# Optimization experiments

Measured on AMD Instinct MI355X. Metric: run time of the kernel, lower is better.

## Reference

```python
import jax, jax.numpy as jnp
import numpy as np
from jax import lax

LAM = 1.0   # risk.distance calls wasserstein with lam=1
ITS = 20    # and its=20
EPS_K = 1e-6


def setup_inputs() -> dict:
    key = jax.random.key(0)
    k1, k2 = jax.random.split(key)
    N, S, D = 4096, 32, 128
    X_ls = jax.random.normal(k1, (N, S, D), dtype=jnp.float32)
    t = jax.random.randint(k2, (N,), 0, 2).astype(jnp.int32)
    return {"X_ls": X_ls, "t": t}


def _pdist2sq(X, Y):
    # squared Euclidean distance between all pairs: [nt, nc]
    C = -2.0 * (X @ Y.T)
    nx = jnp.sum(jnp.square(X), axis=1, keepdims=True)   # [nt,1]
    ny = jnp.sum(jnp.square(Y), axis=1, keepdims=True)   # [nc,1]
    return C + ny.T + nx


def _sinkhorn_step(Xt, Xc, p, lam, its):
    # Xt: [nt, d], Xc: [nc, d]  -> scalar 2*sum(T*Mt)
    nt = jnp.float32(Xt.shape[0])
    nc = jnp.float32(Xc.shape[0])
    M = _pdist2sq(Xt, Xc)                                   # [nt, nc]
    delta = lax.stop_gradient(jnp.max(M))
    eff_lam = lax.stop_gradient(lam / jnp.mean(M))
    # augmented cost matrix Mt: [nt+1, nc+1]
    row = delta * jnp.ones((1, M.shape[1]), M.dtype)
    col = jnp.concatenate([delta * jnp.ones((M.shape[0], 1), M.dtype),
                           jnp.zeros((1, 1), M.dtype)], axis=0)
    Mt = jnp.concatenate([jnp.concatenate([M, row], axis=0), col], axis=1)
    # marginals a: [nt+1,1], b: [nc+1,1]
    a = jnp.concatenate([(p / nt) * jnp.ones((Xt.shape[0], 1), M.dtype),
                         (1.0 - p) * jnp.ones((1, 1), M.dtype)], axis=0)
    b = jnp.concatenate([((1.0 - p) / nc) * jnp.ones((Xc.shape[0], 1), M.dtype),
                         p * jnp.ones((1, 1), M.dtype)], axis=0)
    K = jnp.exp(-eff_lam * Mt) + EPS_K
    ainvK = K / a
    def body(i, u):
        # u^T K -> transpose -> K^T u : [nc+1,1]
        return 1.0 / (ainvK @ (b / (K.T @ u)))
    u = lax.fori_loop(0, its, body, a)
    v = b / (K.T @ u)                                       # [nc+1,1]
    T = u * (v.T * K)                                       # [nt+1, nc+1]
    T = lax.stop_gradient(T)                                # backpropT=False
    return 2.0 * jnp.sum(T * Mt)


def _wasserstein(X_ls, t, lam=LAM, its=ITS):
    # Data-dependent split on treatment (concrete, eager) — matches tf.where+gather.
    t_np = np.asarray(t)
    it_idx = np.nonzero(t_np > 0)[0]
    ic_idx = np.nonzero(t_np < 1)[0]
    p = jnp.float32(t_np.astype(np.float32).mean())          # p_t = np.mean(t)
    Xt_all = jnp.transpose(X_ls[it_idx], (1, 0, 2))          # [S, nt, d]
    Xc_all = jnp.transpose(X_ls[ic_idx], (1, 0, 2))          # [S, nc, d]
    per_step = jax.vmap(lambda Xt, Xc: _sinkhorn_step(Xt, Xc, p, lam, its))
    return jnp.sum(per_step(Xt_all, Xc_all))                 # sum over timesteps


def reference(X_ls, t):
    return _wasserstein(X_ls, t)
```

## Files before the change

### kernel.cpp

```cpp
#include <hip/hip_runtime.h>
#include <stdint.h>

typedef unsigned char u8;
typedef unsigned short u16;
typedef uint32_t u32;

#define NTOT 4096
#define SS   32
#define DD   128
#define EPSK 1e-6f
#define NITER 20
#define CAPC 4460544u
#define LDC_FIT 2304
#define WSTR 2432
#define SU_OFF 2308
#define UNT_OFF 2309
#define BPT 16

typedef __attribute__((ext_vector_type(8))) short short8;
typedef __attribute__((ext_vector_type(4))) float f32x4;
typedef __attribute__((ext_vector_type(2))) float f32x2;

__device__ __forceinline__ float bf2f(u16 h){ return __uint_as_float(((u32)h) << 16); }
__device__ __forceinline__ u16 f2bf(float f){
  u32 u = __float_as_uint(f);
  u += 0x7fffu + ((u >> 16) & 1u);
  return (u16)(u >> 16);
}
__device__ __forceinline__ int invpermc(int cp){
  return (cp & ~63) | ((cp & 3) << 4) | ((cp >> 2) & 15);
}

__global__ __launch_bounds__(1024) void k_compact(const int* __restrict__ t,
    int* __restrict__ itidx, int* __restrict__ icidx, int* __restrict__ meta,
    float* __restrict__ fmeta)
{
  __shared__ int sc[1024];
  int tid = threadIdx.x;
  int e0 = tid * 4;
  int tv[4]; int c = 0;
  #pragma unroll
  for (int e = 0; e < 4; e++){ tv[e] = t[e0 + e]; c += (tv[e] > 0) ? 1 : 0; }
  sc[tid] = c;
  __syncthreads();
  for (int off = 1; off < 1024; off <<= 1){
    int v = sc[tid];
    int add = (tid >= off) ? sc[tid - off] : 0;
    __syncthreads();
    sc[tid] = v + add;
    __syncthreads();
  }
  int incl = sc[tid];
  int excl = incl - c;
  int oT = excl, oC = e0 - excl;
  #pragma unroll
  for (int e = 0; e < 4; e++){
    if (tv[e] > 0) itidx[oT++] = e0 + e;
    else           icidx[oC++] = e0 + e;
  }
  if (tid == 1023){
    meta[0] = incl; meta[1] = NTOT - incl;
    fmeta[0] = (float)incl / (float)NTOT;
  }
}

__global__ void k_zero(float* __restrict__ p, int n)
{
  int i = blockIdx.x * 256 + threadIdx.x;
  if (i < n) p[i] = 0.f;
}

__global__ void k_vinit(const float* __restrict__ fmeta, float* __restrict__ w0)
{
  if (threadIdx.x == 0){
    float p = fmeta[0];
    float* w = w0 + (size_t)blockIdx.x * WSTR;
    w[SU_OFF]  = p;
    w[UNT_OFF] = 1.0f - p;
  }
}

__global__ __launch_bounds__(256) void k_pack(const float* __restrict__ X,
    const int* __restrict__ itidx, const int* __restrict__ icidx,
    const int* __restrict__ meta, u16* __restrict__ XT, u16* __restrict__ XC,
    float* __restrict__ nxT, float* __restrict__ nxC, int ts0)
{
  int r = blockIdx.x * 256 + threadIdx.x;
  int isC = blockIdx.y;
  int z = blockIdx.z;
  int s = ts0 + z;
  int n = isC ? meta[1] : meta[0];
  if (r >= n) return;
  int idx = isC ? icidx[r] : itidx[r];
  const float4* src = (const float4*)(X + ((size_t)idx * SS + s) * DD);
  u16* dst = (isC ? XC : XT) + ((size_t)z * NTOT + r) * DD;
  float nrm = 0.f;
  #pragma unroll
  for (int q = 0; q < 32; q++){
    float4 v = src[q];
    nrm += v.x*v.x + v.y*v.y + v.z*v.z + v.w*v.w;
    u32 lo = (u32)f2bf(v.x) | ((u32)f2bf(v.y) << 16);
    u32 hi = (u32)f2bf(v.z) | ((u32)f2bf(v.w) << 16);
    uint2 pk; pk.x = lo; pk.y = hi;
    ((uint2*)dst)[q] = pk;
  }
  (isC ? nxC : nxT)[z * NTOT + r] = nrm;
}

__global__ __launch_bounds__(256) void k_stats(const u16* __restrict__ XT,
    const u16* __restrict__ XC, const float* __restrict__ nxT, const float* __restrict__ nxC,
    const int* __restrict__ meta, float* __restrict__ gsx, float* __restrict__ gsn)
{
  int side = blockIdx.y, z = blockIdx.z;
  int n = side ? meta[1] : meta[0];
  int chunk = (n + 7) >> 3;
  int r0 = blockIdx.x * chunk;
  int r1 = min(r0 + chunk, n);
  const u16* B = (side ? XC : XT) + (size_t)z * NTOT * DD;
  int tid = threadIdx.x;
  int d = tid & 127, half = tid >> 7;
  float sx = 0.f;
  for (int r = r0 + half; r < r1; r += 2) sx += bf2f(B[(size_t)r * DD + d]);
  __shared__ float sp[256];
  sp[tid] = sx;
  __syncthreads();
  if (tid < 128) unsafeAtomicAdd(&gsx[(size_t)(z*2+side)*128 + tid], sp[tid] + sp[tid+128]);
  const float* nrm = (side ? nxC : nxT) + (size_t)z * NTOT;
  float sn = 0.f;
  for (int r = r0 + tid; r < r1; r += 256) sn += nrm[r];
  #pragma unroll
  for (int o = 32; o; o >>= 1) sn += __shfl_xor(sn, o);
  __syncthreads();
  if ((tid & 63) == 0) sp[tid >> 6] = sn;
  __syncthreads();
  if (tid == 0) unsafeAtomicAdd(&gsn[z*2+side], sp[0]+sp[1]+sp[2]+sp[3]);
}

__global__ void k_lam(const float* __restrict__ gsx, const float* __restrict__ gsn,
                      const int* __restrict__ meta, float* __restrict__ stats)
{
  int z = blockIdx.x, tid = threadIdx.x;
  float d = gsx[(size_t)(z*2)*128 + tid] * gsx[(size_t)(z*2+1)*128 + tid];
  #pragma unroll
  for (int o = 32; o; o >>= 1) d += __shfl_xor(d, o);
  __shared__ float rr[2];
  if ((tid & 63) == 0) rr[tid >> 6] = d;
  __syncthreads();
  if (tid == 0){
    float nt = (float)meta[0], nc = (float)meta[1];
    float msum = nc * gsn[z*2] + nt * gsn[z*2+1] - 2.f * (rr[0] + rr[1]);
    stats[z*8+0] = nt * nc / msum;
    stats[z*8+1] = msum / (nt * nc);
  }
}

#define LDA2 72
__global__ __launch_bounds__(256) void k_gemm(const u16* __restrict__ XT,
    const u16* __restrict__ XC, const float* __restrict__ nxT, const float* __restrict__ nxC,
    const int* __restrict__ meta, const float* __restrict__ fmeta,
    float* __restrict__ stats, u8* __restrict__ Kc, float* __restrict__ w0base)
{
  int nt = meta[0], nc = meta[1];
  if (nt > LDC_FIT || nc > LDC_FIT) return;
  int bx = blockIdx.x, by = blockIdx.y, z = blockIdx.z;
  if (by * 128 >= nt || bx * 128 >= nc) return;
  __shared__ __align__(16) u16 As[128 * LDA2];
  __shared__ __align__(16) u16 Bs[128 * LDA2];
  __shared__ float watile[256];
  __shared__ float nxs[128];
  __shared__ float nys[128];
  int tid = threadIdx.x;
  int wid = tid >> 6, lane = tid & 63;
  int wm = (wid >> 1) * 64, wn = (wid & 1) * 64;
  int lrow = lane & 15, lquad = lane >> 4;

  if (tid < 128){
    int gi = by*128 + tid;
    nxs[tid] = (gi < nt) ? nxT[(size_t)z * NTOT + gi] : 0.f;
  } else {
    int gj = bx*128 + (tid - 128);
    nys[tid - 128] = (gj < nc) ? nxC[(size_t)z * NTOT + gj] : 0.f;
  }

  f32x4 acc[4][4];
  #pragma unroll
  for (int i = 0; i < 4; i++){
    #pragma unroll
    for (int j = 0; j < 4; j++){
      acc[i][j][0]=0.f; acc[i][j][1]=0.f; acc[i][j][2]=0.f; acc[i][j][3]=0.f;
    }
  }

  int r = tid & 127;
  int isB = tid >> 7;
  int g = (isB ? bx : by) * 128 + r;
  int lim = isB ? nc : nt;
  const u16* srcbase = (isB ? XC : XT) + ((size_t)z * NTOT + g) * DD;
  u16* dl = (isB ? Bs : As) + r * LDA2;

  for (int kh = 0; kh < 2; kh++){
    __syncthreads();
    if (g < lim){
      const uint4* src = (const uint4*)(srcbase + kh * 64);
      #pragma unroll
      for (int q = 0; q < 8; q++) ((uint4*)dl)[q] = src[q];
    } else {
      uint4 zz; zz.x=0; zz.y=0; zz.z=0; zz.w=0;
      #pragma unroll
      for (int q = 0; q < 8; q++) ((uint4*)dl)[q] = zz;
    }
    __syncthreads();
    #pragma unroll
    for (int ks = 0; ks < 2; ks++){
      int koff = ks * 32 + lquad * 8;
      short8 af[4], bfr[4];
      #pragma unroll
      for (int i = 0; i < 4; i++) af[i]  = *(const short8*)(As + (wm + i*16 + lrow) * LDA2 + koff);
      #pragma unroll
      for (int j = 0; j < 4; j++) bfr[j] = *(const short8*)(Bs + (wn + j*16 + lrow) * LDA2 + koff);
      #pragma unroll
      for (int i = 0; i < 4; i++){
        #pragma unroll
        for (int j = 0; j < 4; j++){
          acc[i][j] = __builtin_amdgcn_mfma_f32_16x16x32_bf16(af[i], bfr[j], acc[i][j], 0, 0, 0);
        }
      }
    }
  }

  int ldc = (nc + 127) & ~127;
  float lam = stats[z*8+0];
  float p = fmeta[0];
  float a0 = p / (float)nt;
  u8* Kz = Kc + (size_t)z * CAPC;

  float nyv[4]; bool jin[4];
  #pragma unroll
  for (int j = 0; j < 4; j++){
    int lcol = wn + j*16 + lrow;
    jin[j] = (bx*128 + lcol) < nc;
    nyv[j] = nys[lcol];
  }
  float vmax = 0.f;
  float colsum[4] = {0.f, 0.f, 0.f, 0.f};
  size_t cbase = (size_t)(bx*128 + wn + lrow*4);
  #pragma unroll
  for (int i = 0; i < 4; i++){
    #pragma unroll
    for (int rr2 = 0; rr2 < 4; rr2++){
      int lr = wm + i*16 + lquad*4 + rr2;
      int gi = by*128 + lr;
      bool iin = gi < nt;
      float nxv = nxs[lr];
      float cv[4];
      #pragma unroll
      for (int j = 0; j < 4; j++){
        float m = nxv + nyv[j] - 2.0f * acc[i][j][rr2];
        cv[j] = __expf(-lam * m);
        if (iin && jin[j]){ vmax = fmaxf(vmax, m); colsum[j] += cv[j]; }
      }
      u32 pk = (u32)__builtin_amdgcn_cvt_pk_fp8_f32(cv[0], cv[1], 0, false);
      pk = (u32)__builtin_amdgcn_cvt_pk_fp8_f32(cv[2], cv[3], (int)pk, true);
      if (iin) *(u32*)(Kz + (size_t)gi * ldc + cbase) = pk;
    }
  }
  #pragma unroll
  for (int j = 0; j < 4; j++){
    colsum[j] += __shfl_xor(colsum[j], 16);
    colsum[j] += __shfl_xor(colsum[j], 32);
  }
  if (lane < 16){
    #pragma unroll
    for (int j = 0; j < 4; j++) watile[wid * 64 + j*16 + lrow] = colsum[j];
  }
  #pragma unroll
  for (int o = 32; o; o >>= 1) vmax = fmaxf(vmax, __shfl_xor(vmax, o));
  if (lane == 0) atomicMax((int*)stats + z*8 + 2, __float_as_int(vmax));
  __syncthreads();
  if (tid < 128){
    int gj = bx*128 + tid;
    if (gj < nc){
      float v = (tid < 64) ? (watile[tid] + watile[128 + tid])
                           : (watile[64 + (tid-64)] + watile[192 + (tid-64)]);
      unsafeAtomicAdd(w0base + (size_t)z * WSTR + gj, v * a0);
    }
  }
}

__global__ __launch_bounds__(256, 2) void k_iter(const u8* __restrict__ Kc,
    const float* __restrict__ wprev, float* __restrict__ wnext,
    float* __restrict__ ubuf, const int* __restrict__ meta,
    const float* __restrict__ fmeta, const float* __restrict__ stats, int writeU)
{
  __shared__ __align__(16) float zl[LDC_FIT];
  __shared__ __align__(16) float watw[4 * LDC_FIT];
  __shared__ float red[4];
  int nt = meta[0], nc = meta[1];
  if (nt > LDC_FIT || nc > LDC_FIT) return;
  int ldc = (nc + 127) & ~127;
  int z = blockIdx.y, b = blockIdx.x;
  int tid = threadIdx.x, wid = tid >> 6, lane = tid & 63;
  float p = fmeta[0];
  float b0 = (1.0f - p) / (float)nc;
  float a0 = p / (float)nt;
  float lam = stats[z*8+0];
  float delta = stats[z*8+2];
  float kc = __expf(-lam * delta);
  float kce = kc + EPSK;
  const float* wp = wprev + (size_t)z * WSTR;
  float* wnx = wnext + (size_t)z * WSTR;
  float SU = wp[SU_OFF], UNT = wp[UNT_OFF];
  float wext = EPSK * (SU + UNT) + kc * UNT;
  float wnc = kce * SU + (1.0f + EPSK) * UNT;
  float znc = p / wnc;

  float zp = 0.f;
  for (int cp = tid; cp < ldc; cp += 256){
    int c = invpermc(cp);
    float v = 0.f;
    if (c < nc) v = b0 * __builtin_amdgcn_rcpf(wp[c] + wext);
    zl[cp] = v;
    zp += v;
  }
  #pragma unroll
  for (int o = 32; o; o >>= 1) zp += __shfl_xor(zp, o);
  if (lane == 0) red[wid] = zp;
  __syncthreads();
  float Z = red[0] + red[1] + red[2] + red[3];
  float dotX = EPSK * Z + kce * znc;
  float untN = (1.0f - p) / (kce * Z + (1.0f + EPSK) * znc);

  int cb0 = lane * 16;
  float zv[48];
  #pragma unroll
  for (int s = 0; s < 3; s++){
    int cb = s*1024 + cb0;
    if (cb < ldc){
      #pragma unroll
      for (int q = 0; q < 4; q++){
        float4 t4 = *(const float4*)(zl + cb + q*4);
        zv[s*16+q*4+0]=t4.x; zv[s*16+q*4+1]=t4.y; zv[s*16+q*4+2]=t4.z; zv[s*16+q*4+3]=t4.w;
      }
    } else {
      #pragma unroll
      for (int k = 0; k < 16; k++) zv[s*16+k] = 0.f;
    }
  }

  float wacc[48];
  #pragma unroll
  for (int k = 0; k < 48; k++) wacc[k] = 0.f;
  float rsum = 0.f;

  int rpb = (nt + BPT - 1) / BPT;
  int r0 = b * rpb, r1 = min(r0 + rpb, nt);
  const u8* Kz = Kc + (size_t)z * CAPC;

  for (int r = r0 + wid; r < r1; r += 4){
    const u8* Kr = Kz + (size_t)r * ldc;
    uint4 kq[3];
    #pragma unroll
    for (int s = 0; s < 3; s++){
      int cb = s*1024 + cb0;
      if (cb < ldc) kq[s] = *(const uint4*)(Kr + cb);
      else { kq[s].x=0u; kq[s].y=0u; kq[s].z=0u; kq[s].w=0u; }
    }
    float kd[48];
    #pragma unroll
    for (int s = 0; s < 3; s++){
      u32 wd[4] = {kq[s].x, kq[s].y, kq[s].z, kq[s].w};
      #pragma unroll
      for (int q = 0; q < 4; q++){
        f32x2 d0 = __builtin_amdgcn_cvt_pk_f32_fp8((int)wd[q], false);
        f32x2 d1 = __builtin_amdgcn_cvt_pk_f32_fp8((int)wd[q], true);
        kd[s*16+q*4+0] = d0.x; kd[s*16+q*4+1] = d0.y;
        kd[s*16+q*4+2] = d1.x; kd[s*16+q*4+3] = d1.y;
      }
    }
    float d4[4] = {0.f, 0.f, 0.f, 0.f};
    #pragma unroll
    for (int k = 0; k < 48; k++) d4[k & 3] = fmaf(kd[k], zv[k], d4[k & 3]);
    float dot = (d4[0] + d4[1]) + (d4[2] + d4[3]);
    #pragma unroll
    for (int o = 32; o; o >>= 1) dot += __shfl_xor(dot, o);
    float uv = a0 * __builtin_amdgcn_rcpf(dot + dotX);
    rsum += uv;
    if (writeU && lane == 0) ubuf[(size_t)z * WSTR + r] = uv;
    #pragma unroll
    for (int k = 0; k < 48; k++) wacc[k] = fmaf(kd[k], uv, wacc[k]);
  }
  #pragma unroll
  for (int s = 0; s < 3; s++){
    int cb = s*1024 + cb0;
    if (cb < ldc){
      #pragma unroll
      for (int q = 0; q < 4; q++)
        *(float4*)(watw + (size_t)wid * LDC_FIT + cb + q*4) =
            make_float4(wacc[s*16+q*4+0], wacc[s*16+q*4+1], wacc[s*16+q*4+2], wacc[s*16+q*4+3]);
    }
  }
  if (lane == 0) unsafeAtomicAdd(wnx + SU_OFF, rsum);
  if (b == 0 && tid == 0) wnx[UNT_OFF] = untN;
  __syncthreads();
  for (int cp = tid; cp < ldc; cp += 256){
    int c = invpermc(cp);
    if (c < nc){
      float v = watw[cp] + watw[LDC_FIT + cp] + watw[2*LDC_FIT + cp] + watw[3*LDC_FIT + cp];
      unsafeAtomicAdd(wnx + c, v);
    }
  }
}

__global__ __launch_bounds__(256, 2) void k_fin(const u8* __restrict__ Kc,
    const float* __restrict__ wprev, const float* __restrict__ ubuf,
    const int* __restrict__ meta, const float* __restrict__ fmeta,
    const float* __restrict__ stats, float* __restrict__ tsacc, int ts0)
{
  __shared__ __align__(16) float zl[LDC_FIT];
  __shared__ float red[4];
  int nt = meta[0], nc = meta[1];
  if (nt > LDC_FIT || nc > LDC_FIT) return;
  int ldc = (nc + 127) & ~127;
  int z = blockIdx.y, b = blockIdx.x;
  int tid = threadIdx.x, wid = tid >> 6, lane = tid & 63;
  float p = fmeta[0];
  float b0 = (1.0f - p) / (float)nc;
  float lam = stats[z*8+0];
  float invlam = stats[z*8+1];
  float delta = stats[z*8+2];
  float kc = __expf(-lam * delta);
  float kce = kc + EPSK;
  const float* wp = wprev + (size_t)z * WSTR;
  float SU = wp[SU_OFF], UNT = wp[UNT_OFF];
  float wext = EPSK * (SU + UNT) + kc * UNT;
  float wnc = kce * SU + (1.0f + EPSK) * UNT;
  float znc = p / wnc;

  float zp = 0.f;
  for (int cp = tid; cp < ldc; cp += 256){
    int c = invpermc(cp);
    float v = 0.f;
    if (c < nc) v = b0 * __builtin_amdgcn_rcpf(wp[c] + wext);
    zl[cp] = v;
    zp += v;
  }
  #pragma unroll
  for (int o = 32; o; o >>= 1) zp += __shfl_xor(zp, o);
  if (lane == 0) red[wid] = zp;
  __syncthreads();
  float Z = red[0] + red[1] + red[2] + red[3];

  int cb0 = lane * 16;
  float zv[48];
  #pragma unroll
  for (int s = 0; s < 3; s++){
    int cb = s*1024 + cb0;
    if (cb < ldc){
      #pragma unroll
      for (int q = 0; q < 4; q++){
        float4 t4 = *(const float4*)(zl + cb + q*4);
        zv[s*16+q*4+0]=t4.x; zv[s*16+q*4+1]=t4.y; zv[s*16+q*4+2]=t4.z; zv[s*16+q*4+3]=t4.w;
      }
    } else {
      #pragma unroll
      for (int k = 0; k < 16; k++) zv[s*16+k] = 0.f;
    }
  }

  int rpb = (nt + BPT - 1) / BPT;
  int r0 = b * rpb, r1 = min(r0 + rpb, nt);
  const u8* Kz = Kc + (size_t)z * CAPC;
  float wsum = 0.f;

  for (int r = r0 + wid; r < r1; r += 4){
    const u8* Kr = Kz + (size_t)r * ldc;
    float d4[4] = {0.f, 0.f, 0.f, 0.f};
    #pragma unroll
    for (int s = 0; s < 3; s++){
      int cb = s*1024 + cb0;
      if (cb < ldc){
        uint4 kq = *(const uint4*)(Kr + cb);
        u32 wd[4] = {kq.x, kq.y, kq.z, kq.w};
        #pragma unroll
        for (int q = 0; q < 4; q++){
          f32x2 d0 = __builtin_amdgcn_cvt_pk_f32_fp8((int)wd[q], false);
          f32x2 d1 = __builtin_amdgcn_cvt_pk_f32_fp8((int)wd[q], true);
          float cc[4] = {d0.x, d0.y, d1.x, d1.y};
          int k0 = s*16+q*4;
          #pragma unroll
          for (int e = 0; e < 4; e++){
            d4[e] = fmaf((cc[e] + EPSK) * zv[k0+e], __logf(fmaxf(cc[e], 1e-4f)), d4[e]);
          }
        }
      }
    }
    float inner = (d4[0] + d4[1]) + (d4[2] + d4[3]);
    #pragma unroll
    for (int o = 32; o; o >>= 1) inner += __shfl_xor(inner, o);
    wsum += ubuf[(size_t)z * WSTR + r] * inner;
  }
  if (lane == 0) unsafeAtomicAdd(tsacc + ts0 + z, -invlam * wsum);
  if (b == 0 && tid == 0){
    float aug = delta * kce * (UNT * Z + SU * znc);
    unsafeAtomicAdd(tsacc + ts0 + z, aug);
  }
}

__global__ void k_out(const float* __restrict__ tsacc, float* __restrict__ out)
{
  if (threadIdx.x == 0){
    float s = 0.f;
    for (int i = 0; i < SS; i++) s += tsacc[i];
    out[0] = 2.0f * s;
  }
}

extern "C" void kernel_launch(void* const* d_in, const int* in_sizes, int n_in,
                              void* d_out, int out_size, void* d_ws, size_t ws_size,
                              hipStream_t stream)
{
  const float* X = (const float*)d_in[0];
  const int* t = (const int*)d_in[1];

  const size_t PER_TS = 6810000u;
  const size_t FIXED  = 262144u;
  int TSG = 1;
  if (ws_size > FIXED + PER_TS){
    size_t g = (ws_size - FIXED) / PER_TS;
    TSG = (g > SS) ? SS : (int)g;
  }

  char* pp = (char*)d_ws;
  auto alloc = [&](size_t bytes) -> void* {
    void* r = (void*)pp;
    pp += (bytes + 255) & ~(size_t)255;
    return r;
  };
  u8*    Kbuf  = (u8*)alloc((size_t)TSG * CAPC);
  u16*   XT    = (u16*)alloc((size_t)TSG * NTOT * DD * 2);
  u16*   XC    = (u16*)alloc((size_t)TSG * NTOT * DD * 2);
  float* nxT   = (float*)alloc((size_t)TSG * NTOT * 4);
  float* nxC   = (float*)alloc((size_t)TSG * NTOT * 4);
  float* wbuf  = (float*)alloc((size_t)(NITER + 1) * TSG * WSTR * 4);
  float* ubuf  = (float*)alloc((size_t)TSG * WSTR * 4);
  float* auxf  = (float*)alloc((size_t)TSG * 272 * 4);
  int*   itidx = (int*)alloc(NTOT * 4);
  int*   icidx = (int*)alloc(NTOT * 4);
  int*   meta  = (int*)alloc(256);
  float* fmeta = (float*)alloc(256);
  float* tsacc = (float*)alloc(256);

  float* gsx   = auxf;
  float* gsn   = auxf + (size_t)TSG*256;
  float* stats = gsn + (size_t)TSG*2;
  const int auxn = TSG * 266;
  const int wn  = (NITER + 1) * TSG * WSTR;

  k_zero<<<1, 256, 0, stream>>>(tsacc, 64);
  k_compact<<<1, 1024, 0, stream>>>(t, itidx, icidx, meta, fmeta);

  for (int ts0 = 0; ts0 < SS; ts0 += TSG){
    int cnt = SS - ts0; if (cnt > TSG) cnt = TSG;

    k_zero<<<(auxn + 255)/256, 256, 0, stream>>>(auxf, auxn);
    k_zero<<<(wn + 255)/256, 256, 0, stream>>>(wbuf, wn);
    k_vinit<<<cnt, 64, 0, stream>>>(fmeta, wbuf);
    k_pack<<<dim3(16, 2, cnt), 256, 0, stream>>>(X, itidx, icidx, meta, XT, XC, nxT, nxC, ts0);
    k_stats<<<dim3(8, 2, cnt), 256, 0, stream>>>(XT, XC, nxT, nxC, meta, gsx, gsn);
    k_lam<<<cnt, 128, 0, stream>>>(gsx, gsn, meta, stats);
    k_gemm<<<dim3(18, 18, cnt), 256, 0, stream>>>(XT, XC, nxT, nxC, meta, fmeta, stats, Kbuf, wbuf);

    for (int it = 0; it < NITER; it++){
      k_iter<<<dim3(BPT, cnt), 256, 0, stream>>>(Kbuf,
          wbuf + (size_t)it * TSG * WSTR,
          wbuf + (size_t)(it + 1) * TSG * WSTR,
          ubuf, meta, fmeta, stats, (it == NITER - 1) ? 1 : 0);
    }
    k_fin<<<dim3(BPT, cnt), 256, 0, stream>>>(Kbuf,
        wbuf + (size_t)NITER * TSG * WSTR, ubuf, meta, fmeta, stats, tsacc, ts0);
  }
  k_out<<<1, 64, 0, stream>>>(tsacc, (float*)d_out);
}
```

Before: 1.246 ms.

## Load GEMM fragments directly from global memory, clamp K, retune BPT and TSG

The GEMM kernel no longer stages the A and B tiles through shared memory. Each wave now loads its MFMA fragments straight from global memory, which removes the LDS buffers and two barriers per k-half. Separately, BPT doubles from 16 to 32, the timestep group size is capped at 16 instead of 32, and the exp result is clamped to [0,1] before the fp8 conversion. The direct loads skip out-of-range row bounds checks and give up the cross-wave data reuse that LDS provided, and capping TSG may add more passes over the timesteps.

```diff
diff --git a/kernel.cpp b/kernel.cpp
--- a/kernel.cpp
+++ b/kernel.cpp
@@ -15,7 +15,7 @@
 #define WSTR 2432
 #define SU_OFF 2308
 #define UNT_OFF 2309
-#define BPT 16
+#define BPT 32
 
 typedef __attribute__((ext_vector_type(8))) short short8;
 typedef __attribute__((ext_vector_type(4))) float f32x4;
@@ -154,7 +154,6 @@
   }
 }
 
-#define LDA2 72
 __global__ __launch_bounds__(256) void k_gemm(const u16* __restrict__ XT,
     const u16* __restrict__ XC, const float* __restrict__ nxT, const float* __restrict__ nxC,
     const int* __restrict__ meta, const float* __restrict__ fmeta,
@@ -164,8 +163,6 @@
   if (nt > LDC_FIT || nc > LDC_FIT) return;
   int bx = blockIdx.x, by = blockIdx.y, z = blockIdx.z;
   if (by * 128 >= nt || bx * 128 >= nc) return;
-  __shared__ __align__(16) u16 As[128 * LDA2];
-  __shared__ __align__(16) u16 Bs[128 * LDA2];
   __shared__ float watile[256];
   __shared__ float nxs[128];
   __shared__ float nys[128];
@@ -181,6 +178,7 @@
     int gj = bx*128 + (tid - 128);
     nys[tid - 128] = (gj < nc) ? nxC[(size_t)z * NTOT + gj] : 0.f;
   }
+  __syncthreads();
 
   f32x4 acc[4][4];
   #pragma unroll
@@ -191,39 +189,20 @@
     }
   }
 
-  int r = tid & 127;
-  int isB = tid >> 7;
-  int g = (isB ? bx : by) * 128 + r;
-  int lim = isB ? nc : nt;
-  const u16* srcbase = (isB ? XC : XT) + ((size_t)z * NTOT + g) * DD;
-  u16* dl = (isB ? Bs : As) + r * LDA2;
-
-  for (int kh = 0; kh < 2; kh++){
-    __syncthreads();
-    if (g < lim){
-      const uint4* src = (const uint4*)(srcbase + kh * 64);
-      #pragma unroll
-      for (int q = 0; q < 8; q++) ((uint4*)dl)[q] = src[q];
-    } else {
-      uint4 zz; zz.x=0; zz.y=0; zz.z=0; zz.w=0;
-      #pragma unroll
-      for (int q = 0; q < 8; q++) ((uint4*)dl)[q] = zz;
-    }
-    __syncthreads();
-    #pragma unroll
-    for (int ks = 0; ks < 2; ks++){
-      int koff = ks * 32 + lquad * 8;
-      short8 af[4], bfr[4];
-      #pragma unroll
-      for (int i = 0; i < 4; i++) af[i]  = *(const short8*)(As + (wm + i*16 + lrow) * LDA2 + koff);
-      #pragma unroll
-      for (int j = 0; j < 4; j++) bfr[j] = *(const short8*)(Bs + (wn + j*16 + lrow) * LDA2 + koff);
-      #pragma unroll
-      for (int i = 0; i < 4; i++){
-        #pragma unroll
-        for (int j = 0; j < 4; j++){
-          acc[i][j] = __builtin_amdgcn_mfma_f32_16x16x32_bf16(af[i], bfr[j], acc[i][j], 0, 0, 0);
-        }
+  const u16* baseA = XT + ((size_t)z * NTOT + by*128 + wm + lrow) * DD + lquad*8;
+  const u16* baseB = XC + ((size_t)z * NTOT + bx*128 + wn + lrow) * DD + lquad*8;
+  #pragma unroll
+  for (int step = 0; step < 4; step++){
+    short8 af[4], bfr[4];
+    #pragma unroll
+    for (int i = 0; i < 4; i++) af[i]  = *(const short8*)(baseA + i*16*DD + step*32);
+    #pragma unroll
+    for (int j = 0; j < 4; j++) bfr[j] = *(const short8*)(baseB + j*16*DD + step*32);
+    #pragma unroll
+    for (int i = 0; i < 4; i++){
+      #pragma unroll
+      for (int j = 0; j < 4; j++){
+        acc[i][j] = __builtin_amdgcn_mfma_f32_16x16x32_bf16(af[i], bfr[j], acc[i][j], 0, 0, 0);
       }
     }
   }
@@ -256,7 +235,7 @@
       #pragma unroll
       for (int j = 0; j < 4; j++){
         float m = nxv + nyv[j] - 2.0f * acc[i][j][rr2];
-        cv[j] = __expf(-lam * m);
+        cv[j] = fminf(fmaxf(__expf(-lam * m), 0.0f), 1.0f);
         if (iin && jin[j]){ vmax = fmaxf(vmax, m); colsum[j] += cv[j]; }
       }
       u32 pk = (u32)__builtin_amdgcn_cvt_pk_fp8_f32(cv[0], cv[1], 0, false);
@@ -527,7 +506,7 @@
   int TSG = 1;
   if (ws_size > FIXED + PER_TS){
     size_t g = (ws_size - FIXED) / PER_TS;
-    TSG = (g > SS) ? SS : (int)g;
+    TSG = (g > 16) ? 16 : (int)g;
   }
 
   char* pp = (char*)d_ws;
```

After: 1.536 ms. 1.23x slower.
